# Optimization experiments

Measured on AMD Instinct MI355X. Metric: run time of the kernel, lower is better.

Reference implementation:

```python
import jax, jax.numpy as jnp
import numpy as np

LN_EPS = 1e-5
L2_EPS = 1e-6
TAU = 0.07

def _proj(x, W, b, g, be):
    # Linear + LayerNorm (dropout is identity in eval)
    y = x @ W.T + b
    mu = jnp.mean(y, axis=-1, keepdims=True)
    var = jnp.var(y, axis=-1, keepdims=True)
    return (y - mu) * jax.lax.rsqrt(var + LN_EPS) * g + be

def _l2norm(x):
    return x / (jnp.linalg.norm(x, axis=-1, keepdims=True) + L2_EPS)

def setup_inputs() -> dict:
    key = jax.random.key(0)
    ks = iter(jax.random.split(key, 16))
    B, C, D = 2048, 512, 256
    dims = {"text": 1024, "image": 1024, "audio": 512, "tab": 256}
    inp = {}
    for n, d in dims.items():
        inp[f"f_{n}"] = jax.random.normal(next(ks), (B, d), jnp.float32)
        inp[f"W_{n}"] = jax.random.normal(next(ks), (D, d), jnp.float32) * (1.0 / np.sqrt(d))
        inp[f"b_{n}"] = jnp.zeros((D,), jnp.float32)
        inp[f"g_{n}"] = jnp.ones((D,), jnp.float32)
        inp[f"be_{n}"] = jnp.zeros((D,), jnp.float32)
    inp["U"] = jax.random.normal(next(ks), (C, D), jnp.float32) * (1.0 / np.sqrt(D))
    inp["O"] = jax.random.normal(next(ks), (C, D), jnp.float32) * (1.0 / np.sqrt(D))
    inp["cls_bias"] = jnp.zeros((C,), jnp.float32)
    return inp

def reference(f_text, f_image, f_audio, f_tab,
              W_text, b_text, g_text, be_text,
              W_image, b_image, g_image, be_image,
              W_audio, b_audio, g_audio, be_audio,
              W_tab, b_tab, g_tab, be_tab,
              U, O, cls_bias):
    # Per-modality projection -> Z: [B, M, D]
    Z = jnp.stack([
        _proj(f_text, W_text, b_text, g_text, be_text),
        _proj(f_image, W_image, b_image, g_image, be_image),
        _proj(f_audio, W_audio, b_audio, g_audio, be_audio),
        _proj(f_tab, W_tab, b_tab, g_tab, be_tab),
    ], axis=1)
    Zn = _l2norm(Z)            # [B, M, D]
    Un = _l2norm(U)            # [C, D]
    sim = jnp.einsum('bmd,cd->bmc', Zn, Un) / max(TAU, 1e-6)
    r = jax.nn.softmax(sim, axis=1)                 # softmax over modalities M
    Cmix = jnp.einsum('bmc,bmd->bcd', r, Z)         # [B, C, D]
    logits = jnp.einsum('cd,bcd->bc', O, Cmix) + cls_bias
    OjZi = jnp.einsum('cd,bmd->bmc', O, Z)
    contrib = OjZi * r
    return logits, r, sim, contrib
```

## Files before the change

### kernel.cpp

```cpp
#include <hip/hip_runtime.h>
#include <math.h>

typedef __attribute__((ext_vector_type(8))) short short8;
typedef __attribute__((ext_vector_type(4))) float f32x4;
typedef unsigned short ushort_t;

constexpr int Bn = 2048, Mn = 4, Cn = 512, Dn = 256;
constexpr size_t LOGITS_OFF = 0;
constexpr size_t R_OFF   = (size_t)Bn * Cn;
constexpr size_t SIM_OFF = R_OFF + (size_t)Bn * Mn * Cn;
constexpr size_t CTR_OFF = SIM_OFF + (size_t)Bn * Mn * Cn;
constexpr float INV_TAU = 1.0f / 0.07f;

__device__ __forceinline__ unsigned short f2bf(float f) {
  unsigned u = __float_as_uint(f);
  u += 0x7fffu + ((u >> 16) & 1u);
  return (unsigned short)(u >> 16);
}

__device__ __forceinline__ void gload16(const void* g, void* l) {
  __builtin_amdgcn_global_load_lds(
      (const __attribute__((address_space(1))) void*)g,
      (__attribute__((address_space(3))) void*)l, 16, 0, 0);
}

struct CvtArgs {
  const float* src[6];
  ushort_t* dst[6];
  int n[6];
};

__global__ __launch_bounds__(256) void cvt_kernel(CvtArgs a,
                                                  const float* __restrict__ U,
                                                  float* __restrict__ invU) {
  int arr = blockIdx.y;
  if (arr == 6) {
    int c = blockIdx.x * 4 + (threadIdx.x >> 6);
    int lane = threadIdx.x & 63;
    float4 v = *(const float4*)&U[(size_t)c * Dn + lane * 4];
    float s = v.x*v.x + v.y*v.y + v.z*v.z + v.w*v.w;
    #pragma unroll
    for (int m = 32; m >= 1; m >>= 1) s += __shfl_xor(s, m, 64);
    if (lane == 0) invU[c] = 1.0f / (sqrtf(s) + 1e-6f);
    return;
  }
  int idx = (blockIdx.x * 256 + threadIdx.x) * 8;
  if (idx >= a.n[arr]) return;
  const float4* s = (const float4*)(a.src[arr] + idx);
  float4 v0 = s[0], v1 = s[1];
  uint4 p;
  p.x = f2bf(v0.x) | ((unsigned)f2bf(v0.y) << 16);
  p.y = f2bf(v0.z) | ((unsigned)f2bf(v0.w) << 16);
  p.z = f2bf(v1.x) | ((unsigned)f2bf(v1.y) << 16);
  p.w = f2bf(v1.z) | ((unsigned)f2bf(v1.w) << 16);
  *(uint4*)(a.dst[arr] + idx) = p;
}

struct ProjArgs {
  const float* f[4];
  const float* b[4];
  const float* g[4];
  const float* be[4];
  const ushort_t* Wb[4];
  int K[4];
};

__global__ __launch_bounds__(256, 2) void proj_kernel(ProjArgs a,
                                                      ushort_t* __restrict__ Zb,
                                                      float* __restrict__ invZ) {
  const int m = blockIdx.y;
  const int K = a.K[m];
  const float* __restrict__ F = a.f[m];
  const ushort_t* __restrict__ Wm = a.Wb[m];

  const int tid = threadIdx.x;
  const int w = tid >> 6, l = tid & 63;
  const int rg = l >> 4, c16 = l & 15;
  const int row0 = blockIdx.x * 16;

  __shared__ ushort_t aS[2][512];
  __shared__ ushort_t bS[2][8192];
  __shared__ float pS[4][16][2];
  __shared__ float qS[4][16];
  __shared__ ushort_t zS[16][264];

  f32x4 acc[4];
  #pragma unroll
  for (int i = 0; i < 4; i++) acc[i] = (f32x4){0.f, 0.f, 0.f, 0.f};

  const int arow = tid >> 3;
  const int akk  = (tid & 7) * 4;
  const int akc  = akk >> 3, aoff = akk & 7;

  #pragma unroll
  for (int ii = 0; ii < 4; ii++) {
    int i = w + 4 * ii;
    int kc = i >> 2, colblk = i & 3;
    gload16(Wm + (size_t)(colblk * 64 + l) * K + kc * 8,
            &bS[0][(kc * 256 + colblk * 64) * 8]);
  }
  if (tid < 128) {
    float4 v = *(const float4*)(F + (size_t)(row0 + arow) * K + akk);
    uint2 p;
    p.x = f2bf(v.x) | ((unsigned)f2bf(v.y) << 16);
    p.y = f2bf(v.z) | ((unsigned)f2bf(v.w) << 16);
    *(uint2*)&aS[0][(akc * 16 + arow) * 8 + aoff] = p;
  }
  __syncthreads();

  const int NS = K >> 5;
  int cur = 0;
  float4 areg;
  for (int t = 0; t < NS; t++) {
    const int nxt = cur ^ 1;
    const bool more = (t + 1 < NS);
    const int k1 = (t + 1) << 5;
    if (more) {
      #pragma unroll
      for (int ii = 0; ii < 4; ii++) {
        int i = w + 4 * ii;
        int kc = i >> 2, colblk = i & 3;
        gload16(Wm + (size_t)(colblk * 64 + l) * K + k1 + kc * 8,
                &bS[nxt][(kc * 256 + colblk * 64) * 8]);
      }
      if (tid < 128)
        areg = *(const float4*)(F + (size_t)(row0 + arow) * K + k1 + akk);
    }
    short8 av = *(const short8*)&aS[cur][(rg * 16 + c16) * 8];
    #pragma unroll
    for (int nf = 0; nf < 4; nf++) {
      short8 bv = *(const short8*)&bS[cur][(rg * 256 + w * 64 + nf * 16 + c16) * 8];
      acc[nf] = __builtin_amdgcn_mfma_f32_16x16x32_bf16(av, bv, acc[nf], 0, 0, 0);
    }
    if (more && tid < 128) {
      uint2 p;
      p.x = f2bf(areg.x) | ((unsigned)f2bf(areg.y) << 16);
      p.y = f2bf(areg.z) | ((unsigned)f2bf(areg.w) << 16);
      *(uint2*)&aS[nxt][(akc * 16 + arow) * 8 + aoff] = p;
    }
    __syncthreads();
    cur = nxt;
  }

  float bb[4], gg[4], ee[4];
  #pragma unroll
  for (int nf = 0; nf < 4; nf++) {
    int col = w * 64 + nf * 16 + c16;
    bb[nf] = a.b[m][col];
    gg[nf] = a.g[m][col];
    ee[nf] = a.be[m][col];
  }
  float s[4] = {0,0,0,0}, s2[4] = {0,0,0,0};
  #pragma unroll
  for (int nf = 0; nf < 4; nf++)
    #pragma unroll
    for (int j = 0; j < 4; j++) {
      float y = acc[nf][j] + bb[nf];
      acc[nf][j] = y;
      s[j] += y; s2[j] += y * y;
    }
  #pragma unroll
  for (int msk = 8; msk >= 1; msk >>= 1)
    #pragma unroll
    for (int j = 0; j < 4; j++) {
      s[j]  += __shfl_xor(s[j],  msk, 64);
      s2[j] += __shfl_xor(s2[j], msk, 64);
    }
  if (c16 == 0)
    #pragma unroll
    for (int j = 0; j < 4; j++) {
      pS[w][rg*4+j][0] = s[j];
      pS[w][rg*4+j][1] = s2[j];
    }
  __syncthreads();
  float mu[4], rs[4];
  #pragma unroll
  for (int j = 0; j < 4; j++) {
    int row = rg*4 + j;
    float st  = pS[0][row][0] + pS[1][row][0] + pS[2][row][0] + pS[3][row][0];
    float s2t = pS[0][row][1] + pS[1][row][1] + pS[2][row][1] + pS[3][row][1];
    mu[j] = st * (1.0f/256.0f);
    float var = s2t * (1.0f/256.0f) - mu[j]*mu[j];
    rs[j] = rsqrtf(var + 1e-5f);
  }
  float zs[4] = {0,0,0,0};
  #pragma unroll
  for (int nf = 0; nf < 4; nf++)
    #pragma unroll
    for (int j = 0; j < 4; j++) {
      float z = (acc[nf][j] - mu[j]) * rs[j] * gg[nf] + ee[nf];
      acc[nf][j] = z;
      zs[j] += z * z;
    }
  #pragma unroll
  for (int msk = 8; msk >= 1; msk >>= 1)
    #pragma unroll
    for (int j = 0; j < 4; j++) zs[j] += __shfl_xor(zs[j], msk, 64);
  if (c16 == 0)
    #pragma unroll
    for (int j = 0; j < 4; j++) qS[w][rg*4+j] = zs[j];
  __syncthreads();
  #pragma unroll
  for (int j = 0; j < 4; j++) {
    int row = rg*4 + j;
    float zt = qS[0][row] + qS[1][row] + qS[2][row] + qS[3][row];
    float inv = 1.0f / (sqrtf(zt) + 1e-6f);
    if (c16 == 0 && w == 0)
      invZ[(size_t)(row0 + row) * 4 + m] = inv;
  }
  #pragma unroll
  for (int nf = 0; nf < 4; nf++)
    #pragma unroll
    for (int j = 0; j < 4; j++)
      zS[rg*4 + j][w*64 + nf*16 + c16] = f2bf(acc[nf][j]);
  __syncthreads();
  #pragma unroll
  for (int i = 0; i < 2; i++) {
    int c = tid + i * 256;
    int row = c >> 5, colc = (c & 31) * 8;
    uint4 v = *(const uint4*)&zS[row][colc];
    *(uint4*)(Zb + ((size_t)(row0 + row) * 4 + m) * 256 + colc) = v;
  }
}

__global__ __launch_bounds__(256, 4) void dual_kernel(
    const ushort_t* __restrict__ Zb,
    const ushort_t* __restrict__ Ub,
    const ushort_t* __restrict__ Ob,
    const float* __restrict__ invZ, const float* __restrict__ invU,
    const float* __restrict__ cls_bias, float* __restrict__ out) {
  const int tid = threadIdx.x;
  const int w = tid >> 6, l = tid & 63;
  const int wr = w >> 1, wc2 = w & 1;
  const int rg = l >> 4, c16 = l & 15;
  const int row0 = blockIdx.x * 32;
  const int col0 = blockIdx.y * 128;

  __shared__ ushort_t aSd[2][1024];
  __shared__ ushort_t uSd[2][4096];
  __shared__ ushort_t oSd[2][4096];

  f32x4 accU[4], accO[4];
  #pragma unroll
  for (int i = 0; i < 4; i++) {
    accU[i] = (f32x4){0.f, 0.f, 0.f, 0.f};
    accO[i] = (f32x4){0.f, 0.f, 0.f, 0.f};
  }

  auto stage = [&](int buf, int k0) {
    #pragma unroll
    for (int ii = 0; ii < 5; ii++) {
      int i = w + 4 * ii;
      if (i < 2) {
        gload16(Zb + (size_t)(row0 + (l & 31)) * 256 + k0 + ((l >> 5) + i * 2) * 8,
                &aSd[buf][i * 512]);
      } else if (i < 10) {
        int j = i - 2, kc = j >> 1, colblk = j & 1;
        gload16(Ub + (size_t)(col0 + colblk * 64 + l) * 256 + k0 + kc * 8,
                &uSd[buf][(kc * 128 + colblk * 64) * 8]);
      } else if (i < 18) {
        int j = i - 10, kc = j >> 1, colblk = j & 1;
        gload16(Ob + (size_t)(col0 + colblk * 64 + l) * 256 + k0 + kc * 8,
                &oSd[buf][(kc * 128 + colblk * 64) * 8]);
      }
    }
  };

  stage(0, 0);
  __syncthreads();

  int cur = 0;
  #pragma unroll
  for (int t = 0; t < 8; t++) {
    const int nxt = cur ^ 1;
    if (t + 1 < 8) stage(nxt, (t + 1) << 5);
    short8 av = *(const short8*)&aSd[cur][(rg * 32 + wr * 16 + c16) * 8];
    #pragma unroll
    for (int nf = 0; nf < 4; nf++) {
      int chunk = rg * 128 + wc2 * 64 + nf * 16 + c16;
      short8 uv = *(const short8*)&uSd[cur][chunk * 8];
      accU[nf] = __builtin_amdgcn_mfma_f32_16x16x32_bf16(av, uv, accU[nf], 0, 0, 0);
      short8 ov = *(const short8*)&oSd[cur][chunk * 8];
      accO[nf] = __builtin_amdgcn_mfma_f32_16x16x32_bf16(av, ov, accO[nf], 0, 0, 0);
    }
    __syncthreads();
    cur = nxt;
  }

  const int bmb = row0 + wr * 16 + rg * 4;
  const f32x4 iz = *(const f32x4*)&invZ[bmb];
  const int bidx = bmb >> 2;
  #pragma unroll
  for (int nf = 0; nf < 4; nf++) {
    int col = col0 + wc2 * 64 + nf * 16 + c16;
    float iu = invU[col] * INV_TAU;
    f32x4 sU = accU[nf], sO = accO[nf];
    float sim0 = sU[0] * iz[0] * iu;
    float sim1 = sU[1] * iz[1] * iu;
    float sim2 = sU[2] * iz[2] * iu;
    float sim3 = sU[3] * iz[3] * iu;
    float mx = fmaxf(fmaxf(sim0, sim1), fmaxf(sim2, sim3));
    float e0 = __expf(sim0 - mx), e1 = __expf(sim1 - mx);
    float e2 = __expf(sim2 - mx), e3 = __expf(sim3 - mx);
    float rinv = 1.0f / (e0 + e1 + e2 + e3);
    float r0 = e0 * rinv, r1 = e1 * rinv, r2 = e2 * rinv, r3 = e3 * rinv;
    float ct0 = sO[0] * r0, ct1 = sO[1] * r1, ct2 = sO[2] * r2, ct3 = sO[3] * r3;
    size_t sb = (size_t)bmb * Cn + col;
    out[SIM_OFF + sb]        = sim0;
    out[SIM_OFF + sb + Cn]   = sim1;
    out[SIM_OFF + sb + 2*Cn] = sim2;
    out[SIM_OFF + sb + 3*Cn] = sim3;
    out[R_OFF + sb]          = r0;
    out[R_OFF + sb + Cn]     = r1;
    out[R_OFF + sb + 2*Cn]   = r2;
    out[R_OFF + sb + 3*Cn]   = r3;
    out[CTR_OFF + sb]        = ct0;
    out[CTR_OFF + sb + Cn]   = ct1;
    out[CTR_OFF + sb + 2*Cn] = ct2;
    out[CTR_OFF + sb + 3*Cn] = ct3;
    out[LOGITS_OFF + (size_t)bidx * Cn + col] =
        ct0 + ct1 + ct2 + ct3 + cls_bias[col];
  }
}

extern "C" void kernel_launch(void* const* d_in, const int* in_sizes, int n_in,
                              void* d_out, int out_size, void* d_ws, size_t ws_size,
                              hipStream_t stream) {
  const int fi[4] = {0, 5, 10, 15};
  const int Ks[4] = {1024, 1024, 512, 256};

  char* ws = (char*)d_ws;
  ushort_t* Zb  = (ushort_t*)(ws + 0);
  ushort_t* Wb0 = (ushort_t*)(ws + 4194304);
  ushort_t* Wb1 = (ushort_t*)(ws + 4718592);
  ushort_t* Wb2 = (ushort_t*)(ws + 5242880);
  ushort_t* Wb3 = (ushort_t*)(ws + 5505024);
  ushort_t* Ub  = (ushort_t*)(ws + 5636096);
  ushort_t* Ob  = (ushort_t*)(ws + 5898240);
  float* invZ   = (float*)(ws + 6160384);
  float* invU   = (float*)(ws + 6193152);
  ushort_t* Wb[4] = {Wb0, Wb1, Wb2, Wb3};

  ProjArgs pa;
  for (int m = 0; m < 4; m++) {
    pa.f[m]  = (const float*)d_in[fi[m] + 0];
    pa.b[m]  = (const float*)d_in[fi[m] + 2];
    pa.g[m]  = (const float*)d_in[fi[m] + 3];
    pa.be[m] = (const float*)d_in[fi[m] + 4];
    pa.Wb[m] = Wb[m];
    pa.K[m]  = Ks[m];
  }
  const float* U        = (const float*)d_in[20];
  const float* O        = (const float*)d_in[21];
  const float* cls_bias = (const float*)d_in[22];

  CvtArgs ca;
  ca.src[0] = (const float*)d_in[1];   ca.dst[0] = Wb0; ca.n[0] = 262144;
  ca.src[1] = (const float*)d_in[6];   ca.dst[1] = Wb1; ca.n[1] = 262144;
  ca.src[2] = (const float*)d_in[11];  ca.dst[2] = Wb2; ca.n[2] = 131072;
  ca.src[3] = (const float*)d_in[16];  ca.dst[3] = Wb3; ca.n[3] = 65536;
  ca.src[4] = U;                       ca.dst[4] = Ub;  ca.n[4] = 131072;
  ca.src[5] = O;                       ca.dst[5] = Ob;  ca.n[5] = 131072;

  float* out = (float*)d_out;

  cvt_kernel<<<dim3(128, 7), 256, 0, stream>>>(ca, U, invU);
  proj_kernel<<<dim3(Bn / 16, 4), 256, 0, stream>>>(pa, Zb, invZ);
  dual_kernel<<<dim3((Bn * Mn) / 32, Cn / 128), 256, 0, stream>>>(
      Zb, Ub, Ob, invZ, invU, cls_bias, out);
}
```

Measured before the change: 192.3 us.

## Triple-buffer GEMM pipelines with explicit waitcnt, enlarge dual tile, flatten cvt grid

Both the projection and dual GEMM kernels move from double-buffered loops with __syncthreads to triple-buffered prefetch (two stages in flight), using explicit s_waitcnt vmcnt plus raw s_barrier. This lets loads overlap compute without draining the memory queue every step. The dual kernel tile grows to 64 rows per block so each wave reuses U/O fragments across two M-fragments, with occupancy lowered to 2 blocks. The cvt kernel becomes a flat 1D grid with no idle blocks, and the proj A-loads are spread over all 256 threads. The hand-tuned vmcnt(5) values depend on the exact number of loads issued per stage, so any change to the load count can break correctness.

```diff
diff --git a/kernel.cpp b/kernel.cpp
--- a/kernel.cpp
+++ b/kernel.cpp
@@ -3,7 +3,7 @@
 
 typedef __attribute__((ext_vector_type(8))) short short8;
 typedef __attribute__((ext_vector_type(4))) float f32x4;
-typedef unsigned short ushort_t;
+typedef unsigned short u16;
 
 constexpr int Bn = 2048, Mn = 4, Cn = 512, Dn = 256;
 constexpr size_t LOGITS_OFF = 0;
@@ -12,6 +12,9 @@
 constexpr size_t CTR_OFF = SIM_OFF + (size_t)Bn * Mn * Cn;
 constexpr float INV_TAU = 1.0f / 0.07f;
 
+#define WAIT_STEADY asm volatile("s_waitcnt vmcnt(5) lgkmcnt(0)" ::: "memory")
+#define WAIT_LAST   asm volatile("s_waitcnt vmcnt(0) lgkmcnt(0)" ::: "memory")
+
 __device__ __forceinline__ unsigned short f2bf(float f) {
   unsigned u = __float_as_uint(f);
   u += 0x7fffu + ((u >> 16) & 1u);
@@ -26,16 +29,15 @@
 
 struct CvtArgs {
   const float* src[6];
-  ushort_t* dst[6];
-  int n[6];
+  u16* dst[6];
 };
 
 __global__ __launch_bounds__(256) void cvt_kernel(CvtArgs a,
                                                   const float* __restrict__ U,
                                                   float* __restrict__ invU) {
-  int arr = blockIdx.y;
-  if (arr == 6) {
-    int c = blockIdx.x * 4 + (threadIdx.x >> 6);
+  const int blk = blockIdx.x;
+  if (blk >= 480) {
+    int c = (blk - 480) * 4 + (threadIdx.x >> 6);
     int lane = threadIdx.x & 63;
     float4 v = *(const float4*)&U[(size_t)c * Dn + lane * 4];
     float s = v.x*v.x + v.y*v.y + v.z*v.z + v.w*v.w;
@@ -44,16 +46,21 @@
     if (lane == 0) invU[c] = 1.0f / (sqrtf(s) + 1e-6f);
     return;
   }
-  int idx = (blockIdx.x * 256 + threadIdx.x) * 8;
-  if (idx >= a.n[arr]) return;
-  const float4* s = (const float4*)(a.src[arr] + idx);
+  int c = blk * 256 + threadIdx.x;
+  const int ends[6] = {32768, 65536, 81920, 90112, 106496, 122880};
+  int ai = 0, base = 0;
+  #pragma unroll
+  for (int i = 0; i < 5; i++)
+    if (c >= ends[i]) { ai = i + 1; base = ends[i]; }
+  int idx = (c - base) * 8;
+  const float4* s = (const float4*)(a.src[ai] + idx);
   float4 v0 = s[0], v1 = s[1];
   uint4 p;
   p.x = f2bf(v0.x) | ((unsigned)f2bf(v0.y) << 16);
   p.y = f2bf(v0.z) | ((unsigned)f2bf(v0.w) << 16);
   p.z = f2bf(v1.x) | ((unsigned)f2bf(v1.y) << 16);
   p.w = f2bf(v1.z) | ((unsigned)f2bf(v1.w) << 16);
-  *(uint4*)(a.dst[arr] + idx) = p;
+  *(uint4*)(a.dst[ai] + idx) = p;
 }
 
 struct ProjArgs {
@@ -61,85 +68,78 @@
   const float* b[4];
   const float* g[4];
   const float* be[4];
-  const ushort_t* Wb[4];
+  const u16* Wb[4];
   int K[4];
 };
 
 __global__ __launch_bounds__(256, 2) void proj_kernel(ProjArgs a,
-                                                      ushort_t* __restrict__ Zb,
+                                                      u16* __restrict__ Zb,
                                                       float* __restrict__ invZ) {
   const int m = blockIdx.y;
   const int K = a.K[m];
+  const int NS = K >> 5;
   const float* __restrict__ F = a.f[m];
-  const ushort_t* __restrict__ Wm = a.Wb[m];
+  const u16* __restrict__ Wm = a.Wb[m];
 
   const int tid = threadIdx.x;
   const int w = tid >> 6, l = tid & 63;
   const int rg = l >> 4, c16 = l & 15;
   const int row0 = blockIdx.x * 16;
 
-  __shared__ ushort_t aS[2][512];
-  __shared__ ushort_t bS[2][8192];
+  __shared__ u16 aS[3][512];
+  __shared__ u16 bS[3][8192];
   __shared__ float pS[4][16][2];
   __shared__ float qS[4][16];
-  __shared__ ushort_t zS[16][264];
+  __shared__ u16 zS[16][264];
+
+  const int arow = tid >> 4;
+  const int akk  = (tid & 15) * 2;
+  const float* asrc = F + (size_t)(row0 + arow) * K + akk;
+  const int awi = ((akk >> 3) * 16 + arow) * 8 + (akk & 7);
 
   f32x4 acc[4];
   #pragma unroll
   for (int i = 0; i < 4; i++) acc[i] = (f32x4){0.f, 0.f, 0.f, 0.f};
 
-  const int arow = tid >> 3;
-  const int akk  = (tid & 7) * 4;
-  const int akc  = akk >> 3, aoff = akk & 7;
-
-  #pragma unroll
-  for (int ii = 0; ii < 4; ii++) {
-    int i = w + 4 * ii;
-    int kc = i >> 2, colblk = i & 3;
-    gload16(Wm + (size_t)(colblk * 64 + l) * K + kc * 8,
-            &bS[0][(kc * 256 + colblk * 64) * 8]);
-  }
-  if (tid < 128) {
-    float4 v = *(const float4*)(F + (size_t)(row0 + arow) * K + akk);
-    uint2 p;
-    p.x = f2bf(v.x) | ((unsigned)f2bf(v.y) << 16);
-    p.y = f2bf(v.z) | ((unsigned)f2bf(v.w) << 16);
-    *(uint2*)&aS[0][(akc * 16 + arow) * 8 + aoff] = p;
-  }
-  __syncthreads();
-
-  const int NS = K >> 5;
-  int cur = 0;
-  float4 areg;
-  for (int t = 0; t < NS; t++) {
-    const int nxt = cur ^ 1;
-    const bool more = (t + 1 < NS);
-    const int k1 = (t + 1) << 5;
-    if (more) {
-      #pragma unroll
-      for (int ii = 0; ii < 4; ii++) {
-        int i = w + 4 * ii;
-        int kc = i >> 2, colblk = i & 3;
-        gload16(Wm + (size_t)(colblk * 64 + l) * K + k1 + kc * 8,
-                &bS[nxt][(kc * 256 + colblk * 64) * 8]);
-      }
-      if (tid < 128)
-        areg = *(const float4*)(F + (size_t)(row0 + arow) * K + k1 + akk);
-    }
-    short8 av = *(const short8*)&aS[cur][(rg * 16 + c16) * 8];
+  auto bstage = [&](int nb, int k0) {
+    #pragma unroll
+    for (int ii = 0; ii < 4; ii++)
+      gload16(Wm + (size_t)(w * 64 + l) * K + k0 + ii * 8,
+              &bS[nb][(ii * 256 + w * 64) * 8]);
+  };
+  auto aload = [&](int t) -> float2 {
+    return *(const float2*)(asrc + ((size_t)t << 5));
+  };
+  auto awrite = [&](int nb, float2 v) {
+    unsigned p = f2bf(v.x) | ((unsigned)f2bf(v.y) << 16);
+    *(unsigned*)&aS[nb][awi] = p;
+  };
+  auto compute = [&](int cb) {
+    short8 av = *(const short8*)&aS[cb][(rg * 16 + c16) * 8];
     #pragma unroll
     for (int nf = 0; nf < 4; nf++) {
-      short8 bv = *(const short8*)&bS[cur][(rg * 256 + w * 64 + nf * 16 + c16) * 8];
+      short8 bv = *(const short8*)&bS[cb][(rg * 256 + w * 64 + nf * 16 + c16) * 8];
       acc[nf] = __builtin_amdgcn_mfma_f32_16x16x32_bf16(av, bv, acc[nf], 0, 0, 0);
     }
-    if (more && tid < 128) {
-      uint2 p;
-      p.x = f2bf(areg.x) | ((unsigned)f2bf(areg.y) << 16);
-      p.y = f2bf(areg.z) | ((unsigned)f2bf(areg.w) << 16);
-      *(uint2*)&aS[nxt][(akc * 16 + arow) * 8 + aoff] = p;
-    }
-    __syncthreads();
-    cur = nxt;
+  };
+
+  float2 aA = aload(0);
+  bstage(0, 0);
+  float2 aB = aload(1);
+  bstage(1, 32);
+  awrite(0, aA);
+
+  for (int tt = 0; tt < NS; tt += 2) {
+    WAIT_STEADY;
+    __builtin_amdgcn_s_barrier();
+    if (tt + 2 < NS) { aA = aload(tt + 2); bstage((tt + 2) % 3, (tt + 2) << 5); }
+    awrite((tt + 1) % 3, aB);
+    compute(tt % 3);
+    if (tt < NS - 2) WAIT_STEADY; else WAIT_LAST;
+    __builtin_amdgcn_s_barrier();
+    if (tt + 3 < NS) { aB = aload(tt + 3); bstage((tt + 3) % 3, (tt + 3) << 5); }
+    if (tt + 2 < NS) awrite((tt + 2) % 3, aA);
+    compute((tt + 1) % 3);
   }
 
   float bb[4], gg[4], ee[4];
@@ -223,103 +223,103 @@
   }
 }
 
-__global__ __launch_bounds__(256, 4) void dual_kernel(
-    const ushort_t* __restrict__ Zb,
-    const ushort_t* __restrict__ Ub,
-    const ushort_t* __restrict__ Ob,
+__global__ __launch_bounds__(256, 2) void dual_kernel(
+    const u16* __restrict__ Zb,
+    const u16* __restrict__ Ub,
+    const u16* __restrict__ Ob,
     const float* __restrict__ invZ, const float* __restrict__ invU,
     const float* __restrict__ cls_bias, float* __restrict__ out) {
   const int tid = threadIdx.x;
   const int w = tid >> 6, l = tid & 63;
   const int wr = w >> 1, wc2 = w & 1;
   const int rg = l >> 4, c16 = l & 15;
-  const int row0 = blockIdx.x * 32;
+  const int row0 = blockIdx.x * 64;
   const int col0 = blockIdx.y * 128;
 
-  __shared__ ushort_t aSd[2][1024];
-  __shared__ ushort_t uSd[2][4096];
-  __shared__ ushort_t oSd[2][4096];
-
-  f32x4 accU[4], accO[4];
-  #pragma unroll
-  for (int i = 0; i < 4; i++) {
-    accU[i] = (f32x4){0.f, 0.f, 0.f, 0.f};
-    accO[i] = (f32x4){0.f, 0.f, 0.f, 0.f};
-  }
-
-  auto stage = [&](int buf, int k0) {
-    #pragma unroll
-    for (int ii = 0; ii < 5; ii++) {
-      int i = w + 4 * ii;
-      if (i < 2) {
-        gload16(Zb + (size_t)(row0 + (l & 31)) * 256 + k0 + ((l >> 5) + i * 2) * 8,
-                &aSd[buf][i * 512]);
-      } else if (i < 10) {
-        int j = i - 2, kc = j >> 1, colblk = j & 1;
-        gload16(Ub + (size_t)(col0 + colblk * 64 + l) * 256 + k0 + kc * 8,
-                &uSd[buf][(kc * 128 + colblk * 64) * 8]);
-      } else if (i < 18) {
-        int j = i - 10, kc = j >> 1, colblk = j & 1;
-        gload16(Ob + (size_t)(col0 + colblk * 64 + l) * 256 + k0 + kc * 8,
-                &oSd[buf][(kc * 128 + colblk * 64) * 8]);
-      }
-    }
-  };
-
-  stage(0, 0);
-  __syncthreads();
-
-  int cur = 0;
-  #pragma unroll
-  for (int t = 0; t < 8; t++) {
-    const int nxt = cur ^ 1;
-    if (t + 1 < 8) stage(nxt, (t + 1) << 5);
-    short8 av = *(const short8*)&aSd[cur][(rg * 32 + wr * 16 + c16) * 8];
+  __shared__ u16 aS[3][2048];
+  __shared__ u16 uS[3][4096];
+  __shared__ u16 oS[3][4096];
+
+  f32x4 accU[2][4], accO[2][4];
+  #pragma unroll
+  for (int i = 0; i < 2; i++)
+    #pragma unroll
+    for (int j = 0; j < 4; j++) {
+      accU[i][j] = (f32x4){0.f, 0.f, 0.f, 0.f};
+      accO[i][j] = (f32x4){0.f, 0.f, 0.f, 0.f};
+    }
+
+  auto stage = [&](int nb, int k0) {
+    gload16(Zb + (size_t)(row0 + l) * 256 + k0 + w * 8, &aS[nb][w * 512]);
+    #pragma unroll
+    for (int jj = 0; jj < 2; jj++) {
+      gload16(Ub + (size_t)(col0 + jj * 64 + l) * 256 + k0 + w * 8,
+              &uS[nb][(w * 128 + jj * 64) * 8]);
+      gload16(Ob + (size_t)(col0 + jj * 64 + l) * 256 + k0 + w * 8,
+              &oS[nb][(w * 128 + jj * 64) * 8]);
+    }
+  };
+  auto compute = [&](int cb) {
+    short8 av0 = *(const short8*)&aS[cb][(rg * 64 + wr * 32 + c16) * 8];
+    short8 av1 = *(const short8*)&aS[cb][(rg * 64 + wr * 32 + 16 + c16) * 8];
     #pragma unroll
     for (int nf = 0; nf < 4; nf++) {
       int chunk = rg * 128 + wc2 * 64 + nf * 16 + c16;
-      short8 uv = *(const short8*)&uSd[cur][chunk * 8];
-      accU[nf] = __builtin_amdgcn_mfma_f32_16x16x32_bf16(av, uv, accU[nf], 0, 0, 0);
-      short8 ov = *(const short8*)&oSd[cur][chunk * 8];
-      accO[nf] = __builtin_amdgcn_mfma_f32_16x16x32_bf16(av, ov, accO[nf], 0, 0, 0);
-    }
-    __syncthreads();
-    cur = nxt;
-  }
-
-  const int bmb = row0 + wr * 16 + rg * 4;
-  const f32x4 iz = *(const f32x4*)&invZ[bmb];
-  const int bidx = bmb >> 2;
-  #pragma unroll
-  for (int nf = 0; nf < 4; nf++) {
-    int col = col0 + wc2 * 64 + nf * 16 + c16;
-    float iu = invU[col] * INV_TAU;
-    f32x4 sU = accU[nf], sO = accO[nf];
-    float sim0 = sU[0] * iz[0] * iu;
-    float sim1 = sU[1] * iz[1] * iu;
-    float sim2 = sU[2] * iz[2] * iu;
-    float sim3 = sU[3] * iz[3] * iu;
-    float mx = fmaxf(fmaxf(sim0, sim1), fmaxf(sim2, sim3));
-    float e0 = __expf(sim0 - mx), e1 = __expf(sim1 - mx);
-    float e2 = __expf(sim2 - mx), e3 = __expf(sim3 - mx);
-    float rinv = 1.0f / (e0 + e1 + e2 + e3);
-    float r0 = e0 * rinv, r1 = e1 * rinv, r2 = e2 * rinv, r3 = e3 * rinv;
-    float ct0 = sO[0] * r0, ct1 = sO[1] * r1, ct2 = sO[2] * r2, ct3 = sO[3] * r3;
-    size_t sb = (size_t)bmb * Cn + col;
-    out[SIM_OFF + sb]        = sim0;
-    out[SIM_OFF + sb + Cn]   = sim1;
-    out[SIM_OFF + sb + 2*Cn] = sim2;
-    out[SIM_OFF + sb + 3*Cn] = sim3;
-    out[R_OFF + sb]          = r0;
-    out[R_OFF + sb + Cn]     = r1;
-    out[R_OFF + sb + 2*Cn]   = r2;
-    out[R_OFF + sb + 3*Cn]   = r3;
-    out[CTR_OFF + sb]        = ct0;
-    out[CTR_OFF + sb + Cn]   = ct1;
-    out[CTR_OFF + sb + 2*Cn] = ct2;
-    out[CTR_OFF + sb + 3*Cn] = ct3;
-    out[LOGITS_OFF + (size_t)bidx * Cn + col] =
-        ct0 + ct1 + ct2 + ct3 + cls_bias[col];
+      short8 uv = *(const short8*)&uS[cb][chunk * 8];
+      accU[0][nf] = __builtin_amdgcn_mfma_f32_16x16x32_bf16(av0, uv, accU[0][nf], 0, 0, 0);
+      accU[1][nf] = __builtin_amdgcn_mfma_f32_16x16x32_bf16(av1, uv, accU[1][nf], 0, 0, 0);
+      short8 ov = *(const short8*)&oS[cb][chunk * 8];
+      accO[0][nf] = __builtin_amdgcn_mfma_f32_16x16x32_bf16(av0, ov, accO[0][nf], 0, 0, 0);
+      accO[1][nf] = __builtin_amdgcn_mfma_f32_16x16x32_bf16(av1, ov, accO[1][nf], 0, 0, 0);
+    }
+  };
+
+  stage(0, 0);
+  stage(1, 32);
+  #pragma unroll
+  for (int t = 0; t < 8; t++) {
+    if (t < 7) WAIT_STEADY; else WAIT_LAST;
+    __builtin_amdgcn_s_barrier();
+    if (t + 2 < 8) stage((t + 2) % 3, (t + 2) << 5);
+    compute(t % 3);
+  }
+
+  #pragma unroll
+  for (int mf = 0; mf < 2; mf++) {
+    const int bmb = row0 + wr * 32 + mf * 16 + rg * 4;
+    const f32x4 iz = *(const f32x4*)&invZ[bmb];
+    const int bidx = bmb >> 2;
+    #pragma unroll
+    for (int nf = 0; nf < 4; nf++) {
+      int col = col0 + wc2 * 64 + nf * 16 + c16;
+      float iu = invU[col] * INV_TAU;
+      f32x4 sU = accU[mf][nf], sO = accO[mf][nf];
+      float sim0 = sU[0] * iz[0] * iu;
+      float sim1 = sU[1] * iz[1] * iu;
+      float sim2 = sU[2] * iz[2] * iu;
+      float sim3 = sU[3] * iz[3] * iu;
+      float mx = fmaxf(fmaxf(sim0, sim1), fmaxf(sim2, sim3));
+      float e0 = __expf(sim0 - mx), e1 = __expf(sim1 - mx);
+      float e2 = __expf(sim2 - mx), e3 = __expf(sim3 - mx);
+      float rinv = 1.0f / (e0 + e1 + e2 + e3);
+      float r0 = e0 * rinv, r1 = e1 * rinv, r2 = e2 * rinv, r3 = e3 * rinv;
+      float ct0 = sO[0] * r0, ct1 = sO[1] * r1, ct2 = sO[2] * r2, ct3 = sO[3] * r3;
+      size_t sb = (size_t)bmb * Cn + col;
+      out[SIM_OFF + sb]        = sim0;
+      out[SIM_OFF + sb + Cn]   = sim1;
+      out[SIM_OFF + sb + 2*Cn] = sim2;
+      out[SIM_OFF + sb + 3*Cn] = sim3;
+      out[R_OFF + sb]          = r0;
+      out[R_OFF + sb + Cn]     = r1;
+      out[R_OFF + sb + 2*Cn]   = r2;
+      out[R_OFF + sb + 3*Cn]   = r3;
+      out[CTR_OFF + sb]        = ct0;
+      out[CTR_OFF + sb + Cn]   = ct1;
+      out[CTR_OFF + sb + 2*Cn] = ct2;
+      out[CTR_OFF + sb + 3*Cn] = ct3;
+      out[LOGITS_OFF + (size_t)bidx * Cn + col] =
+          ct0 + ct1 + ct2 + ct3 + cls_bias[col];
+    }
   }
 }
 
@@ -330,16 +330,16 @@
   const int Ks[4] = {1024, 1024, 512, 256};
 
   char* ws = (char*)d_ws;
-  ushort_t* Zb  = (ushort_t*)(ws + 0);
-  ushort_t* Wb0 = (ushort_t*)(ws + 4194304);
-  ushort_t* Wb1 = (ushort_t*)(ws + 4718592);
-  ushort_t* Wb2 = (ushort_t*)(ws + 5242880);
-  ushort_t* Wb3 = (ushort_t*)(ws + 5505024);
-  ushort_t* Ub  = (ushort_t*)(ws + 5636096);
-  ushort_t* Ob  = (ushort_t*)(ws + 5898240);
-  float* invZ   = (float*)(ws + 6160384);
-  float* invU   = (float*)(ws + 6193152);
-  ushort_t* Wb[4] = {Wb0, Wb1, Wb2, Wb3};
+  u16* Zb  = (u16*)(ws + 0);
+  u16* Wb0 = (u16*)(ws + 4194304);
+  u16* Wb1 = (u16*)(ws + 4718592);
+  u16* Wb2 = (u16*)(ws + 5242880);
+  u16* Wb3 = (u16*)(ws + 5505024);
+  u16* Ub  = (u16*)(ws + 5636096);
+  u16* Ob  = (u16*)(ws + 5898240);
+  float* invZ = (float*)(ws + 6160384);
+  float* invU = (float*)(ws + 6193152);
+  u16* Wb[4] = {Wb0, Wb1, Wb2, Wb3};
 
   ProjArgs pa;
   for (int m = 0; m < 4; m++) {
@@ -355,17 +355,17 @@
   const float* cls_bias = (const float*)d_in[22];
 
   CvtArgs ca;
-  ca.src[0] = (const float*)d_in[1];   ca.dst[0] = Wb0; ca.n[0] = 262144;
-  ca.src[1] = (const float*)d_in[6];   ca.dst[1] = Wb1; ca.n[1] = 262144;
-  ca.src[2] = (const float*)d_in[11];  ca.dst[2] = Wb2; ca.n[2] = 131072;
-  ca.src[3] = (const float*)d_in[16];  ca.dst[3] = Wb3; ca.n[3] = 65536;
-  ca.src[4] = U;                       ca.dst[4] = Ub;  ca.n[4] = 131072;
-  ca.src[5] = O;                       ca.dst[5] = Ob;  ca.n[5] = 131072;
+  ca.src[0] = (const float*)d_in[1];   ca.dst[0] = Wb0;
+  ca.src[1] = (const float*)d_in[6];   ca.dst[1] = Wb1;
+  ca.src[2] = (const float*)d_in[11];  ca.dst[2] = Wb2;
+  ca.src[3] = (const float*)d_in[16];  ca.dst[3] = Wb3;
+  ca.src[4] = U;                       ca.dst[4] = Ub;
+  ca.src[5] = O;                       ca.dst[5] = Ob;
 
   float* out = (float*)d_out;
 
-  cvt_kernel<<<dim3(128, 7), 256, 0, stream>>>(ca, U, invU);
+  cvt_kernel<<<608, 256, 0, stream>>>(ca, U, invU);
   proj_kernel<<<dim3(Bn / 16, 4), 256, 0, stream>>>(pa, Zb, invZ);
-  dual_kernel<<<dim3((Bn * Mn) / 32, Cn / 128), 256, 0, stream>>>(
+  dual_kernel<<<dim3((Bn * Mn) / 64, Cn / 128), 256, 0, stream>>>(
       Zb, Ub, Ob, invZ, invU, cls_bias, out);
 }
```

New measurement: 180.1 us. 6.3% less time.
